# Kernel tuning notes

Measured on AMD Instinct MI355X. Metric: run time of the kernel, lower is better.

The kernel has to match this reference:

```python
import jax, jax.numpy as jnp
import numpy as np

SCOPE = 27
RICKER_WIDTH = 6.0
DAMPING = 0.12
IN_CHANNELS = 256


def _ricker(scope, std, damping):
    # mexican-hat / ricker wavelet, length `scope`, centered
    x = jnp.arange(scope, dtype=jnp.float32) - (scope // 2)
    a = 2.0 / (jnp.sqrt(3.0 * std) * jnp.pi ** 0.25)
    return damping * a * (1.0 - (x / std) ** 2) * jnp.exp(-(x ** 2) / (2.0 * std ** 2))


def _pad_roll(k, in_channels):
    # zero-pad kernel (length scope) to in_channels, roll so center sits at i=0-ish
    scope = k.shape[-1]
    pad_left = (in_channels - scope) // 2
    pad_right = in_channels - scope - pad_left
    padded = jnp.concatenate([jnp.zeros((pad_left,), k.dtype), k, jnp.zeros((pad_right,), k.dtype)])
    return jnp.roll(padded, in_channels // 2 + 1)


def _circulant(kernel, c):
    # tpl[i, j] = kernel[(j - i) mod C]  (each row is the kernel rolled by i)
    idx = (jnp.arange(c)[None, :] - jnp.arange(c)[:, None]) % c
    return kernel[idx]


def setup_inputs() -> dict:
    key = jax.random.key(0)
    k1, _ = jax.random.split(key)
    activations = jax.random.normal(k1, (32, IN_CHANNELS, 64, 64), dtype=jnp.float32)
    inhibition_filter = _ricker(SCOPE, RICKER_WIDTH, DAMPING)  # learned param, ricker init
    return {"activations": activations, "inhibition_filter": inhibition_filter}


def reference(activations, inhibition_filter):
    n, c, h, w = activations.shape
    kernel = _pad_roll(inhibition_filter, c)              # [C]
    tpl = _circulant(kernel, c)                           # [C, C]
    tpl_inv = jnp.linalg.inv(jnp.eye(c, dtype=tpl.dtype) - tpl)  # [C, C]
    # torch: (N, H*W, C) @ tpl_inv -> out[n, c_out, h, w] = sum_k act[n, k, h, w] * tpl_inv[k, c_out]
    return jnp.einsum('nkhw,kc->nchw', activations, tpl_inv)
```

## Files before the change

kernel.cpp:

```cpp
#include <hip/hip_runtime.h>
#include <hip/hip_bf16.h>

#define C 256
#define HW 4096
#define REP_ROW 288
#define LDSK 264

typedef __attribute__((ext_vector_type(8))) short short8;
typedef __attribute__((ext_vector_type(4))) float float4v;

__device__ __forceinline__ unsigned short f2bf(float x) {
    unsigned u = __builtin_bit_cast(unsigned, x);
    u = (u + 0x7fffu + ((u >> 16) & 1u)) >> 16;
    return (unsigned short)u;
}

__global__ void build_rep_kernel(const float* __restrict__ filt, unsigned short* __restrict__ rep) {
    __shared__ float twc[256], tws[256];
    __shared__ float Gre[256], Gim[256];
    __shared__ float gsh[256];
    const int t = threadIdx.x;
    const double PI = 3.14159265358979323846;
    double th = (double)t * (PI / 128.0);
    twc[t] = (float)cos(th);
    tws[t] = (float)sin(th);
    __syncthreads();
    float re = 1.0f, im = 0.0f;
    for (int i = 0; i < 27; ++i) {
        int d = (243 + i) & 255;
        int idx = (t * d) & 255;
        float fv = filt[i];
        re -= fv * twc[idx];
        im += fv * tws[idx];
    }
    float den = re * re + im * im;
    Gre[t] = re / den;
    Gim[t] = -im / den;
    __syncthreads();
    float acc = 0.0f;
    for (int f = 0; f < 256; ++f) {
        int idx = (f * t) & 255;
        acc += Gre[f] * twc[idx] - Gim[f] * tws[idx];
    }
    gsh[t] = acc * (1.0f / 256.0f);
    __syncthreads();
    for (int e = t; e < 8 * REP_ROW; e += 256) {
        int row = e / REP_ROW, u = e - row * REP_ROW;
        int src = (16 - u - row) & 255;
        rep[e] = f2bf(gsh[src]);
    }
}

__global__ __launch_bounds__(256, 3)
void toeplitz_gemm_kernel(const float* __restrict__ act,
                          const unsigned short* __restrict__ rep_g,
                          float* __restrict__ out) {
    __shared__ unsigned short rep2[8 * REP_ROW];
    __shared__ unsigned short atile[64 * LDSK];

    const int tid = threadIdx.x;
    const int wave = tid >> 6;
    const int lane = tid & 63;
    const int m = lane & 15;
    const int quad = lane >> 4;
    const int blk = blockIdx.x;
    const int n = blk >> 6;
    const int p0 = (blk & 63) << 6;
    const float* actn = act + (size_t)n * (C * HW);
    float* outn = out + (size_t)n * (C * HW);

    {
        const uint4* rg = (const uint4*)rep_g;
        uint4* rl = (uint4*)rep2;
        for (int i = tid; i < (8 * REP_ROW * 2) / 16; i += 256) rl[i] = rg[i];
    }

    {
        const int kb = (tid & 15) << 2;
        const int pb = (tid >> 4) << 2;
#pragma unroll
        for (int half = 0; half < 2; ++half) {
            float4v r[8];
#pragma unroll
            for (int it = 0; it < 2; ++it) {
                const int ks = (half * 2 + it) * 64 + kb;
                const float* g0 = actn + (size_t)ks * HW + p0 + pb;
#pragma unroll
                for (int j = 0; j < 4; ++j)
                    r[it * 4 + j] = *(const float4v*)(g0 + (size_t)j * HW);
            }
#pragma unroll
            for (int it = 0; it < 2; ++it) {
                const int ks = (half * 2 + it) * 64 + kb;
#pragma unroll
                for (int pp = 0; pp < 4; ++pp) {
                    unsigned long long pk =
                          (unsigned long long)f2bf(r[it * 4 + 0][pp])
                        | ((unsigned long long)f2bf(r[it * 4 + 1][pp]) << 16)
                        | ((unsigned long long)f2bf(r[it * 4 + 2][pp]) << 32)
                        | ((unsigned long long)f2bf(r[it * 4 + 3][pp]) << 48);
                    *(unsigned long long*)&atile[(pb + pp) * LDSK + ks] = pk;
                }
            }
        }
    }
    __syncthreads();

    const int arow = (-m) & 7;
    const int abase = arow * 287 + 16 + quad * 8 - m;

    float4v acc[4][4];
#pragma unroll
    for (int ct = 0; ct < 4; ++ct)
#pragma unroll
        for (int pt = 0; pt < 4; ++pt)
            acc[ct][pt] = (float4v){0.f, 0.f, 0.f, 0.f};

#pragma unroll
    for (int a = 0; a < 8; ++a) {
        const int k0 = a * 32;
        short8 bfr[4];
#pragma unroll
        for (int pt = 0; pt < 4; ++pt) {
            const int prow = pt * 16 + m;
            bfr[pt] = *(const short8*)&atile[prow * LDSK + k0 + quad * 8];
        }
        short8 afr[4];
#pragma unroll
        for (int ct = 0; ct < 4; ++ct) {
            const int f = (2 * a - ct) & 15;
            const int sp = (f - 4 * wave) & 15;
            afr[ct] = *(const short8*)&rep2[abase + (sp << 4)];
        }
#pragma unroll
        for (int ct = 0; ct < 4; ++ct) {
#pragma unroll
            for (int pt = 0; pt < 4; ++pt) {
                acc[ct][pt] = __builtin_amdgcn_mfma_f32_16x16x32_bf16(
                    afr[ct], bfr[pt], acc[ct][pt], 0, 0, 0);
            }
        }
    }

#pragma unroll
    for (int ct = 0; ct < 4; ++ct) {
#pragma unroll
        for (int r = 0; r < 4; ++r) {
            const int c = wave * 64 + ct * 16 + quad * 4 + r;
            float* op = outn + (size_t)c * HW + p0;
#pragma unroll
            for (int pt = 0; pt < 4; ++pt) {
                op[pt * 16 + m] = acc[ct][pt][r];
            }
        }
    }
}

extern "C" void kernel_launch(void* const* d_in, const int* in_sizes, int n_in,
                              void* d_out, int out_size, void* d_ws, size_t ws_size,
                              hipStream_t stream) {
    const float* act = (const float*)d_in[0];
    const float* filt = (const float*)d_in[1];
    float* out = (float*)d_out;
    unsigned short* rep = (unsigned short*)d_ws;

    build_rep_kernel<<<1, 256, 0, stream>>>(filt, rep);
    toeplitz_gemm_kernel<<<2048, 256, 0, stream>>>(act, rep, out);
}
```

Measured before the change: 256.2 us.

## Stream activation chunks via async global-to-LDS loads with double buffering

Replaces the upfront register-staged load and bf16 conversion of the whole 256-channel activation tile with four 64-channel chunks. Each chunk is loaded as raw fp32 straight into a double-buffered LDS area using global_load_lds, so loading the next chunk overlaps MFMA work on the current one. Conversion to bf16 now happens at fragment-build time, using a simpler round-half-up rounding instead of round-to-nearest-even. The circulant table is precomputed in per-lane fragment order so A fragments come from LDS with a direct index. The trade-off is extra scalar LDS reads and conversion in the inner loop, dword-granularity async loads, and added barriers.

New measurement: 250.4 us. 2.3% less time.

```diff
diff --git a/kernel.cpp b/kernel.cpp
--- a/kernel.cpp
+++ b/kernel.cpp
@@ -3,8 +3,7 @@
 
 #define C 256
 #define HW 4096
-#define REP_ROW 288
-#define LDSK 264
+#define CHUNK_STRIDE 66
 
 typedef __attribute__((ext_vector_type(8))) short short8;
 typedef __attribute__((ext_vector_type(4))) float float4v;
@@ -15,7 +14,18 @@
     return (unsigned short)u;
 }
 
-__global__ void build_rep_kernel(const float* __restrict__ filt, unsigned short* __restrict__ rep) {
+__device__ __forceinline__ void g2l_b32(const void* g, void* l) {
+    __builtin_amdgcn_global_load_lds(
+        (const __attribute__((address_space(1))) unsigned int*)g,
+        (__attribute__((address_space(3))) unsigned int*)l, 4, 0, 0);
+}
+__device__ __forceinline__ void g2l_b128(const void* g, void* l) {
+    __builtin_amdgcn_global_load_lds(
+        (const __attribute__((address_space(1))) unsigned int*)g,
+        (__attribute__((address_space(3))) unsigned int*)l, 16, 0, 0);
+}
+
+__global__ void build_tab_kernel(const float* __restrict__ filt, unsigned short* __restrict__ tab) {
     __shared__ float twc[256], tws[256];
     __shared__ float Gre[256], Gim[256];
     __shared__ float gsh[256];
@@ -44,19 +54,22 @@
     }
     gsh[t] = acc * (1.0f / 256.0f);
     __syncthreads();
-    for (int e = t; e < 8 * REP_ROW; e += 256) {
-        int row = e / REP_ROW, u = e - row * REP_ROW;
-        int src = (16 - u - row) & 255;
-        rep[e] = f2bf(gsh[src]);
+    for (int e = t; e < 16 * 64 * 8; e += 256) {
+        int j = e & 7;
+        int lane = (e >> 3) & 63;
+        int s = e >> 9;
+        int m = lane & 15, q = lane >> 4;
+        int src = (m - 16 * s - 8 * q - j) & 255;
+        tab[e] = f2bf(gsh[src]);
     }
 }
 
 __global__ __launch_bounds__(256, 3)
 void toeplitz_gemm_kernel(const float* __restrict__ act,
-                          const unsigned short* __restrict__ rep_g,
+                          const unsigned short* __restrict__ tab,
                           float* __restrict__ out) {
-    __shared__ unsigned short rep2[8 * REP_ROW];
-    __shared__ unsigned short atile[64 * LDSK];
+    __shared__ float chunkbuf[2][64 * CHUNK_STRIDE];
+    __shared__ unsigned short afrags[16 * 64 * 8];
 
     const int tid = threadIdx.x;
     const int wave = tid >> 6;
@@ -69,45 +82,19 @@
     const float* actn = act + (size_t)n * (C * HW);
     float* outn = out + (size_t)n * (C * HW);
 
-    {
-        const uint4* rg = (const uint4*)rep_g;
-        uint4* rl = (uint4*)rep2;
-        for (int i = tid; i < (8 * REP_ROW * 2) / 16; i += 256) rl[i] = rg[i];
+#pragma unroll
+    for (int i = 0; i < 4; ++i) {
+        const int seg = wave * 4 + i;
+        g2l_b128(tab + seg * 512 + lane * 8, &afrags[seg * 512]);
     }
 
     {
-        const int kb = (tid & 15) << 2;
-        const int pb = (tid >> 4) << 2;
+        const float* src0 = actn + (size_t)(wave * 16) * HW + p0 + lane;
 #pragma unroll
-        for (int half = 0; half < 2; ++half) {
-            float4v r[8];
-#pragma unroll
-            for (int it = 0; it < 2; ++it) {
-                const int ks = (half * 2 + it) * 64 + kb;
-                const float* g0 = actn + (size_t)ks * HW + p0 + pb;
-#pragma unroll
-                for (int j = 0; j < 4; ++j)
-                    r[it * 4 + j] = *(const float4v*)(g0 + (size_t)j * HW);
-            }
-#pragma unroll
-            for (int it = 0; it < 2; ++it) {
-                const int ks = (half * 2 + it) * 64 + kb;
-#pragma unroll
-                for (int pp = 0; pp < 4; ++pp) {
-                    unsigned long long pk =
-                          (unsigned long long)f2bf(r[it * 4 + 0][pp])
-                        | ((unsigned long long)f2bf(r[it * 4 + 1][pp]) << 16)
-                        | ((unsigned long long)f2bf(r[it * 4 + 2][pp]) << 32)
-                        | ((unsigned long long)f2bf(r[it * 4 + 3][pp]) << 48);
-                    *(unsigned long long*)&atile[(pb + pp) * LDSK + ks] = pk;
-                }
-            }
-        }
+        for (int i = 0; i < 16; ++i)
+            g2l_b32(src0 + (size_t)i * HW, &chunkbuf[0][(wave * 16 + i) * CHUNK_STRIDE]);
     }
     __syncthreads();
-
-    const int arow = (-m) & 7;
-    const int abase = arow * 287 + 16 + quad * 8 - m;
 
     float4v acc[4][4];
 #pragma unroll
@@ -116,38 +103,52 @@
         for (int pt = 0; pt < 4; ++pt)
             acc[ct][pt] = (float4v){0.f, 0.f, 0.f, 0.f};
 
+    for (int c = 0; c < 4; ++c) {
+        if (c < 3) {
+            const float* srcn = actn + (size_t)((c + 1) * 64 + wave * 16) * HW + p0 + lane;
 #pragma unroll
-    for (int a = 0; a < 8; ++a) {
-        const int k0 = a * 32;
-        short8 bfr[4];
+            for (int i = 0; i < 16; ++i)
+                g2l_b32(srcn + (size_t)i * HW, &chunkbuf[(c + 1) & 1][(wave * 16 + i) * CHUNK_STRIDE]);
+        }
+
+        const float* cb = chunkbuf[c & 1];
 #pragma unroll
-        for (int pt = 0; pt < 4; ++pt) {
-            const int prow = pt * 16 + m;
-            bfr[pt] = *(const short8*)&atile[prow * LDSK + k0 + quad * 8];
-        }
-        short8 afr[4];
-#pragma unroll
-        for (int ct = 0; ct < 4; ++ct) {
-            const int f = (2 * a - ct) & 15;
-            const int sp = (f - 4 * wave) & 15;
-            afr[ct] = *(const short8*)&rep2[abase + (sp << 4)];
-        }
-#pragma unroll
-        for (int ct = 0; ct < 4; ++ct) {
+        for (int half = 0; half < 2; ++half) {
+            const int ag = c * 2 + half;
+            short8 bfr[4];
 #pragma unroll
             for (int pt = 0; pt < 4; ++pt) {
-                acc[ct][pt] = __builtin_amdgcn_mfma_f32_16x16x32_bf16(
-                    afr[ct], bfr[pt], acc[ct][pt], 0, 0, 0);
+                const float* base = cb + (half * 32 + quad * 8) * CHUNK_STRIDE + pt * 16 + m;
+                unsigned u[8];
+#pragma unroll
+                for (int j = 0; j < 8; ++j)
+                    u[j] = __builtin_bit_cast(unsigned, base[j * CHUNK_STRIDE]) + 0x8000u;
+                uint4 pk;
+                pk.x = (u[0] >> 16) | (u[1] & 0xFFFF0000u);
+                pk.y = (u[2] >> 16) | (u[3] & 0xFFFF0000u);
+                pk.z = (u[4] >> 16) | (u[5] & 0xFFFF0000u);
+                pk.w = (u[6] >> 16) | (u[7] & 0xFFFF0000u);
+                bfr[pt] = __builtin_bit_cast(short8, pk);
+            }
+#pragma unroll
+            for (int ct = 0; ct < 4; ++ct) {
+                const int sp = ((2 * ag - ct) - 4 * wave) & 15;
+                const short8 af = *(const short8*)&afrags[sp * 512 + lane * 8];
+#pragma unroll
+                for (int pt = 0; pt < 4; ++pt)
+                    acc[ct][pt] = __builtin_amdgcn_mfma_f32_16x16x32_bf16(
+                        af, bfr[pt], acc[ct][pt], 0, 0, 0);
             }
         }
+        if (c < 3) __syncthreads();
     }
 
 #pragma unroll
     for (int ct = 0; ct < 4; ++ct) {
 #pragma unroll
         for (int r = 0; r < 4; ++r) {
-            const int c = wave * 64 + ct * 16 + quad * 4 + r;
-            float* op = outn + (size_t)c * HW + p0;
+            const int cc = wave * 64 + ct * 16 + quad * 4 + r;
+            float* op = outn + (size_t)cc * HW + p0;
 #pragma unroll
             for (int pt = 0; pt < 4; ++pt) {
                 op[pt * 16 + m] = acc[ct][pt][r];
@@ -162,8 +163,8 @@
     const float* act = (const float*)d_in[0];
     const float* filt = (const float*)d_in[1];
     float* out = (float*)d_out;
-    unsigned short* rep = (unsigned short*)d_ws;
+    unsigned short* tab = (unsigned short*)d_ws;
 
-    build_rep_kernel<<<1, 256, 0, stream>>>(filt, rep);
-    toeplitz_gemm_kernel<<<2048, 256, 0, stream>>>(act, rep, out);
+    build_tab_kernel<<<1, 256, 0, stream>>>(filt, tab);
+    toeplitz_gemm_kernel<<<2048, 256, 0, stream>>>(act, tab, out);
 }
```
